# Kernel tuning notes

Hardware: AMD Instinct MI355X
Metric: run time of the kernel (lower is better)

Reference implementation:

```python
import jax, jax.numpy as jnp
import numpy as np

EMBED = 768
HEADS = 12


def setup_inputs() -> dict:
    key = jax.random.key(0)
    k1, k2, k3 = jax.random.split(key, 3)
    B, N, E = 2, 2048, EMBED
    x = jax.random.normal(k1, (B, N, E), dtype=jnp.float32)
    w_qkv = jax.random.normal(k2, (3 * E, E), dtype=jnp.float32) * (1.0 / np.sqrt(E))
    b_qkv = jnp.zeros((3 * E,), dtype=jnp.float32)
    w_o = jax.random.normal(k3, (E, E), dtype=jnp.float32) * (1.0 / np.sqrt(E))
    b_o = jnp.zeros((E,), dtype=jnp.float32)
    return {"x": x, "w_qkv": w_qkv, "b_qkv": b_qkv, "w_o": w_o, "b_o": b_o}


def reference(x, w_qkv, b_qkv, w_o, b_o):
    B, N, E = x.shape
    H = HEADS
    d = E // H
    # fused qkv projection (torch Linear: x @ W^T + b)
    qkv = x @ w_qkv.T + b_qkv                       # [B, N, 3E]
    # Rearrange 'b n (h qkv e) -> b qkv h n e'
    qkv = qkv.reshape(B, N, H, 3, d).transpose(0, 3, 2, 1, 4)  # [B, 3, H, N, d]
    q, k, v = qkv[:, 0], qkv[:, 1], qkv[:, 2]       # each [B, H, N, d]
    scores = jnp.einsum("bhqd,bhkd->bhqk", q, k)    # [B, H, N, N]
    attn = jax.nn.softmax(scores / jnp.sqrt(jnp.float32(E)), axis=-1)
    ctx = jnp.einsum("bhqk,bhkd->bhqd", attn, v)    # [B, H, N, d]
    ctx = ctx.transpose(0, 2, 1, 3).reshape(B, N, E)  # 'b h n d -> b n (h d)'
    out = ctx @ w_o.T + b_o
    return out
```

## Files before the change

### kernel.cpp

```cpp
#include <hip/hip_runtime.h>

#define BB 2
#define NN 2048
#define EE 768
#define HH 12
#define DD 64
#define MM (BB*NN)
#define E3 (3*EE)
#define QSCALE 0.05205877280961602f

typedef __bf16 bf16x8 __attribute__((ext_vector_type(8)));
typedef float  f32x4  __attribute__((ext_vector_type(4)));
typedef unsigned short u16x8 __attribute__((ext_vector_type(8)));

#define MFMA(a,b,c) __builtin_amdgcn_mfma_f32_16x16x32_bf16(a,b,c,0,0,0)

__device__ __forceinline__ unsigned short f2bf(float f) {
    unsigned int u = __float_as_uint(f);
    u += 0x7FFFu + ((u >> 16) & 1u);
    return (unsigned short)(u >> 16);
}

typedef __attribute__((address_space(3))) unsigned int as3u32;
typedef __attribute__((address_space(1))) unsigned int as1u32;
__device__ __forceinline__ void gll16(const void* g, void* l) {
    __builtin_amdgcn_global_load_lds((const as1u32*)(uintptr_t)g,
                                     (as3u32*)(unsigned int)(uintptr_t)l, 16, 0, 0);
}

__global__ __launch_bounds__(256)
void cast_bf16(const float* __restrict__ s, unsigned short* __restrict__ d, int n4) {
    int i = blockIdx.x * 256 + threadIdx.x;
    if (i < n4) {
        float4 v = ((const float4*)s)[i];
        ushort4 o;
        o.x = f2bf(v.x); o.y = f2bf(v.y); o.z = f2bf(v.z); o.w = f2bf(v.w);
        ((ushort4*)d)[i] = o;
    }
}

template<int MODE>
__global__ __launch_bounds__(256)
void gemm_bf16(const unsigned short* __restrict__ A, const unsigned short* __restrict__ W,
               const float* __restrict__ bias,
               unsigned short* __restrict__ o0, unsigned short* __restrict__ o1,
               unsigned short* __restrict__ o2, float* __restrict__ of, int Kd)
{
    __shared__ unsigned short As[128 * 32];
    __shared__ unsigned short Bs[128 * 32];

    const int tid = threadIdx.x;
    const int l = tid & 63;
    const int w = tid >> 6;
    const int m0 = blockIdx.x * 128;
    const int c0 = blockIdx.y * 128;
    const int wm = (w >> 1) * 64;
    const int wn = (w & 1) * 64;

    const int s0 = w * 2;
    const unsigned short* a_src0 = A + (size_t)(m0 + s0*16      + (l>>2)) * Kd + (l&3)*8;
    const unsigned short* a_src1 = A + (size_t)(m0 + (s0+1)*16  + (l>>2)) * Kd + (l&3)*8;
    const unsigned short* b_src0 = W + (size_t)(c0 + s0*16      + (l>>2)) * Kd + (l&3)*8;
    const unsigned short* b_src1 = W + (size_t)(c0 + (s0+1)*16  + (l>>2)) * Kd + (l&3)*8;
    unsigned short* a_dst0 = &As[s0*512];
    unsigned short* a_dst1 = &As[(s0+1)*512];
    unsigned short* b_dst0 = &Bs[s0*512];
    unsigned short* b_dst1 = &Bs[(s0+1)*512];

    const f32x4 zero4 = {0.f, 0.f, 0.f, 0.f};
    f32x4 acc[4][4];
    #pragma unroll
    for (int i = 0; i < 4; ++i)
        #pragma unroll
        for (int j = 0; j < 4; ++j) acc[i][j] = zero4;

    for (int k0 = 0; k0 < Kd; k0 += 32) {
        __syncthreads();
        gll16(a_src0 + k0, a_dst0);
        gll16(a_src1 + k0, a_dst1);
        gll16(b_src0 + k0, b_dst0);
        gll16(b_src1 + k0, b_dst1);
        __syncthreads();

        bf16x8 af[4], bf[4];
        #pragma unroll
        for (int i = 0; i < 4; ++i)
            af[i] = *(const bf16x8*)&As[(wm + 16*i + (l&15))*32 + (l>>4)*8];
        #pragma unroll
        for (int j = 0; j < 4; ++j)
            bf[j] = *(const bf16x8*)&Bs[(wn + 16*j + (l&15))*32 + (l>>4)*8];
        #pragma unroll
        for (int i = 0; i < 4; ++i)
            #pragma unroll
            for (int j = 0; j < 4; ++j)
                acc[i][j] = MFMA(af[i], bf[j], acc[i][j]);
    }

    if (MODE == 0) {
        #pragma unroll
        for (int j = 0; j < 4; ++j) {
            const int col = c0 + wn + 16*j + (l&15);
            const float bj = bias[col];
            #pragma unroll
            for (int i = 0; i < 4; ++i) {
                #pragma unroll
                for (int r = 0; r < 4; ++r) {
                    const int row = m0 + wm + 16*i + (l>>4)*4 + r;
                    of[(size_t)row * EE + col] = acc[i][j][r] + bj;
                }
            }
        }
    } else {
        const int sec = (c0 + wn) >> 6;
        const int hh = sec / 3;
        const int tt = sec - hh*3;
        #pragma unroll
        for (int j = 0; j < 4; ++j) {
            const int col = c0 + wn + 16*j + (l&15);
            const int dcol = 16*j + (l&15);
            const float bj = bias[col];
            #pragma unroll
            for (int i = 0; i < 4; ++i) {
                const int row0 = m0 + wm + 16*i + (l>>4)*4;
                const int b = row0 >> 11;
                const int n = row0 & (NN - 1);
                if (tt == 2) {
                    ushort4 pk;
                    pk.x = f2bf(acc[i][j][0] + bj);
                    pk.y = f2bf(acc[i][j][1] + bj);
                    pk.z = f2bf(acc[i][j][2] + bj);
                    pk.w = f2bf(acc[i][j][3] + bj);
                    *(ushort4*)&o2[(((size_t)b*HH + hh)*DD + dcol)*NN + n] = pk;
                } else {
                    unsigned short* dst = (tt == 0) ? o0 : o1;
                    #pragma unroll
                    for (int r = 0; r < 4; ++r) {
                        float val = acc[i][j][r] + bj;
                        if (tt == 0) val *= QSCALE;
                        dst[(((size_t)b*HH + hh)*NN + n + r)*DD + dcol] = f2bf(val);
                    }
                }
            }
        }
    }
}

__global__ __launch_bounds__(256)
void attn_mfma(const unsigned short* __restrict__ Q, const unsigned short* __restrict__ K,
               const unsigned short* __restrict__ Vt_g, unsigned short* __restrict__ ctx)
{
    __shared__ unsigned short Ks[64 * 72];
    __shared__ unsigned short Vt[64 * 72];
    __shared__ unsigned short Pq[4 * 16 * 72];

    const int tid = threadIdx.x;
    const int l = tid & 63;
    const int w = tid >> 6;
    const int quad = l >> 4;
    const int lc = l & 15;
    const int bq = blockIdx.x, h = blockIdx.y, b = blockIdx.z;
    const size_t hb = ((size_t)(b*HH + h)) * NN * DD;

    const f32x4 zero4 = {0.f, 0.f, 0.f, 0.f};

    const int qrow = bq*64 + w*16 + lc;
    const bf16x8 qf0 = *(const bf16x8*)(Q + hb + (size_t)qrow*DD +      quad*8);
    const bf16x8 qf1 = *(const bf16x8*)(Q + hb + (size_t)qrow*DD + 32 + quad*8);

    f32x4 o[4];
    #pragma unroll
    for (int dj = 0; dj < 4; ++dj) o[dj] = zero4;
    float lsum = 0.f;

    const int srow = tid >> 2;
    const int sc = tid & 3;
    const unsigned short* kbase = K + hb + (size_t)srow*DD + sc*16;
    const unsigned short* vbase = Vt_g + ((size_t)(b*HH + h)*DD + srow)*NN + sc*16;
    unsigned short* ksl = &Ks[srow*72 + sc*16];
    unsigned short* vsl = &Vt[srow*72 + sc*16];

    for (int kt = 0; kt < NN/64; ++kt) {
        const unsigned short* ksrc = kbase + (size_t)kt*64*DD;
        const unsigned short* vsrc = vbase + kt*64;
        u16x8 k0 = *(const u16x8*)ksrc;
        u16x8 k1 = *(const u16x8*)(ksrc + 8);
        u16x8 v0 = *(const u16x8*)vsrc;
        u16x8 v1 = *(const u16x8*)(vsrc + 8);
        __syncthreads();
        *(u16x8*)ksl = k0;
        *(u16x8*)(ksl + 8) = k1;
        *(u16x8*)vsl = v0;
        *(u16x8*)(vsl + 8) = v1;
        __syncthreads();

        f32x4 st[4];
        #pragma unroll
        for (int jf = 0; jf < 4; ++jf) {
            bf16x8 kf0 = *(const bf16x8*)&Ks[(16*jf + lc)*72 +      quad*8];
            bf16x8 kf1 = *(const bf16x8*)&Ks[(16*jf + lc)*72 + 32 + quad*8];
            f32x4 acc0 = MFMA(kf0, qf0, zero4);
            st[jf] = MFMA(kf1, qf1, acc0);
        }

        #pragma unroll
        for (int jf = 0; jf < 4; ++jf) {
            float e0 = __builtin_amdgcn_exp2f(st[jf][0]);
            float e1 = __builtin_amdgcn_exp2f(st[jf][1]);
            float e2 = __builtin_amdgcn_exp2f(st[jf][2]);
            float e3 = __builtin_amdgcn_exp2f(st[jf][3]);
            lsum += (e0 + e1) + (e2 + e3);
            ushort4 pk;
            pk.x = f2bf(e0); pk.y = f2bf(e1); pk.z = f2bf(e2); pk.w = f2bf(e3);
            *(ushort4*)&Pq[w*1152 + lc*72 + 16*jf + quad*4] = pk;
        }

        #pragma unroll
        for (int kb = 0; kb < 2; ++kb) {
            bf16x8 pf = *(const bf16x8*)&Pq[w*1152 + lc*72 + kb*32 + quad*8];
            #pragma unroll
            for (int dj = 0; dj < 4; ++dj) {
                bf16x8 vf = *(const bf16x8*)&Vt[(16*dj + lc)*72 + kb*32 + quad*8];
                o[dj] = MFMA(vf, pf, o[dj]);
            }
        }
    }

    lsum += __shfl_xor(lsum, 16);
    lsum += __shfl_xor(lsum, 32);
    const float inv = 1.f / lsum;

    const int n = bq*64 + w*16 + lc;
    #pragma unroll
    for (int dj = 0; dj < 4; ++dj) {
        ushort4 pk;
        pk.x = f2bf(o[dj][0] * inv);
        pk.y = f2bf(o[dj][1] * inv);
        pk.z = f2bf(o[dj][2] * inv);
        pk.w = f2bf(o[dj][3] * inv);
        *(ushort4*)&ctx[((size_t)(b*NN + n))*EE + h*DD + 16*dj + quad*4] = pk;
    }
}

extern "C" void kernel_launch(void* const* d_in, const int* in_sizes, int n_in,
                              void* d_out, int out_size, void* d_ws, size_t ws_size,
                              hipStream_t stream)
{
    const float* x     = (const float*)d_in[0];
    const float* w_qkv = (const float*)d_in[1];
    const float* b_qkv = (const float*)d_in[2];
    const float* w_o   = (const float*)d_in[3];
    const float* b_o   = (const float*)d_in[4];
    float* out = (float*)d_out;

    unsigned short* wsu = (unsigned short*)d_ws;
    const size_t XB = (size_t)MM * EE;
    const size_t WQ = (size_t)E3 * EE;
    const size_t WO = (size_t)EE * EE;
    const size_t HS = (size_t)BB * HH * NN * DD;
    unsigned short* xb   = wsu;
    unsigned short* wqb  = xb  + XB;
    unsigned short* wob  = wqb + WQ;
    unsigned short* qb   = wob + WO;
    unsigned short* kb   = qb  + HS;
    unsigned short* vtb  = kb  + HS;
    unsigned short* ctxb = vtb + HS;

    cast_bf16<<<(int)((XB/4 + 255)/256), 256, 0, stream>>>(x, xb, (int)(XB/4));
    cast_bf16<<<(int)((WQ/4 + 255)/256), 256, 0, stream>>>(w_qkv, wqb, (int)(WQ/4));
    cast_bf16<<<(int)((WO/4 + 255)/256), 256, 0, stream>>>(w_o, wob, (int)(WO/4));

    dim3 g1(MM/128, E3/128);
    gemm_bf16<1><<<g1, 256, 0, stream>>>(xb, wqb, b_qkv, qb, kb, vtb, nullptr, EE);

    dim3 g2(NN/64, HH, BB);
    attn_mfma<<<g2, 256, 0, stream>>>(qb, kb, vtb, ctxb);

    dim3 g3(MM/128, EE/128);
    gemm_bf16<0><<<g3, 256, 0, stream>>>(ctxb, wob, b_o, nullptr, nullptr, nullptr, out, EE);
}
```

Before: 180.3 us.

## Rewrite attention with 32x32 MFMA, register P shuffles, async LDS loads; fuse casts

Attention now uses 32x32x16 bf16 MFMA with 2 waves per 64-query block, each wave owning 32 queries. The probability tile is repacked to bf16 and passed between lanes with shuffles instead of a round-trip through shared memory. K and V tiles are staged with global_load_lds into XOR-swizzled LDS without padding, and the grid is flattened so the 24 batch-head pairs vary fastest. The three cast kernels are merged into one launch, which relies on xb, wqb and wob being contiguous in the workspace. Fewer threads per block reduce parallel loads, and the loads are still not double-buffered, so latency may stay exposed.

Result: slower. 237.9 us (+31.9%).

```diff
diff --git a/kernel.cpp b/kernel.cpp
--- a/kernel.cpp
+++ b/kernel.cpp
@@ -11,9 +11,12 @@
 
 typedef __bf16 bf16x8 __attribute__((ext_vector_type(8)));
 typedef float  f32x4  __attribute__((ext_vector_type(4)));
+typedef float  f32x16 __attribute__((ext_vector_type(16)));
 typedef unsigned short u16x8 __attribute__((ext_vector_type(8)));
-
-#define MFMA(a,b,c) __builtin_amdgcn_mfma_f32_16x16x32_bf16(a,b,c,0,0,0)
+typedef unsigned int   u32x4 __attribute__((ext_vector_type(4)));
+
+#define MFMA(a,b,c)   __builtin_amdgcn_mfma_f32_16x16x32_bf16(a,b,c,0,0,0)
+#define MFMA32(a,b,c) __builtin_amdgcn_mfma_f32_32x32x16_bf16(a,b,c,0,0,0)
 
 __device__ __forceinline__ unsigned short f2bf(float f) {
     unsigned int u = __float_as_uint(f);
@@ -28,15 +31,22 @@
                                      (as3u32*)(unsigned int)(uintptr_t)l, 16, 0, 0);
 }
 
+#define XB4 786432
+#define WQ4 442368
+#define WO4 147456
 __global__ __launch_bounds__(256)
-void cast_bf16(const float* __restrict__ s, unsigned short* __restrict__ d, int n4) {
+void cast3(const float* __restrict__ x, const float* __restrict__ wq,
+           const float* __restrict__ wo, unsigned short* __restrict__ dst) {
     int i = blockIdx.x * 256 + threadIdx.x;
-    if (i < n4) {
-        float4 v = ((const float4*)s)[i];
-        ushort4 o;
-        o.x = f2bf(v.x); o.y = f2bf(v.y); o.z = f2bf(v.z); o.w = f2bf(v.w);
-        ((ushort4*)d)[i] = o;
-    }
+    const float* src;
+    int off;
+    if (i < XB4)            { src = x;  off = i; }
+    else if (i < XB4+WQ4)   { src = wq; off = i - XB4; }
+    else                    { src = wo; off = i - XB4 - WQ4; }
+    float4 v = ((const float4*)src)[off];
+    ushort4 o;
+    o.x = f2bf(v.x); o.y = f2bf(v.y); o.z = f2bf(v.z); o.w = f2bf(v.w);
+    ((ushort4*)dst)[i] = o;
 }
 
 template<int MODE>
@@ -145,99 +155,115 @@
     }
 }
 
-__global__ __launch_bounds__(256)
+__global__ __launch_bounds__(128)
 void attn_mfma(const unsigned short* __restrict__ Q, const unsigned short* __restrict__ K,
                const unsigned short* __restrict__ Vt_g, unsigned short* __restrict__ ctx)
 {
-    __shared__ unsigned short Ks[64 * 72];
-    __shared__ unsigned short Vt[64 * 72];
-    __shared__ unsigned short Pq[4 * 16 * 72];
+    __shared__ unsigned short Ks[64 * 64];
+    __shared__ unsigned short Vt[64 * 64];
 
     const int tid = threadIdx.x;
-    const int l = tid & 63;
-    const int w = tid >> 6;
-    const int quad = l >> 4;
-    const int lc = l & 15;
-    const int bq = blockIdx.x, h = blockIdx.y, b = blockIdx.z;
-    const size_t hb = ((size_t)(b*HH + h)) * NN * DD;
-
-    const f32x4 zero4 = {0.f, 0.f, 0.f, 0.f};
-
-    const int qrow = bq*64 + w*16 + lc;
-    const bf16x8 qf0 = *(const bf16x8*)(Q + hb + (size_t)qrow*DD +      quad*8);
-    const bf16x8 qf1 = *(const bf16x8*)(Q + hb + (size_t)qrow*DD + 32 + quad*8);
-
-    f32x4 o[4];
+    const int l  = tid & 63;
+    const int wv = tid >> 6;
+    const int hf = l >> 5;
+    const int lc = l & 31;
+    const int l7 = l & 7;
+
+    const int id = blockIdx.x;
+    const int bh = id % 24;
+    const int qt = id / 24;
+    const int b  = bh / 12;
+    const int hh = bh - b*12;
+    const size_t hbK = (size_t)bh * NN * DD;
+
+    const f32x16 z16 = {0.f,0.f,0.f,0.f,0.f,0.f,0.f,0.f,
+                        0.f,0.f,0.f,0.f,0.f,0.f,0.f,0.f};
+
+    const int qbase = qt*64 + wv*32;
+    const unsigned short* qptr = Q + hbK + (size_t)(qbase + lc)*DD + hf*8;
+    bf16x8 qf[4];
     #pragma unroll
-    for (int dj = 0; dj < 4; ++dj) o[dj] = zero4;
+    for (int t = 0; t < 4; ++t) qf[t] = *(const bf16x8*)(qptr + t*16);
+
+    const int lr3 = l >> 3;
+    const int cx  = (l & 7) ^ (lr3 & 7);
+    const unsigned short* srcK0 = K   + hbK + (size_t)(32*wv + lr3)*DD + cx*8;
+    const unsigned short* srcV0 = Vt_g + ((size_t)bh*DD + 32*wv + lr3)*NN + cx*8;
+
+    f32x16 o0 = z16, o1 = z16;
     float lsum = 0.f;
 
-    const int srow = tid >> 2;
-    const int sc = tid & 3;
-    const unsigned short* kbase = K + hb + (size_t)srow*DD + sc*16;
-    const unsigned short* vbase = Vt_g + ((size_t)(b*HH + h)*DD + srow)*NN + sc*16;
-    unsigned short* ksl = &Ks[srow*72 + sc*16];
-    unsigned short* vsl = &Vt[srow*72 + sc*16];
-
     for (int kt = 0; kt < NN/64; ++kt) {
-        const unsigned short* ksrc = kbase + (size_t)kt*64*DD;
-        const unsigned short* vsrc = vbase + kt*64;
-        u16x8 k0 = *(const u16x8*)ksrc;
-        u16x8 k1 = *(const u16x8*)(ksrc + 8);
-        u16x8 v0 = *(const u16x8*)vsrc;
-        u16x8 v1 = *(const u16x8*)(vsrc + 8);
         __syncthreads();
-        *(u16x8*)ksl = k0;
-        *(u16x8*)(ksl + 8) = k1;
-        *(u16x8*)vsl = v0;
-        *(u16x8*)(vsl + 8) = v1;
+        const unsigned short* sk = srcK0 + (size_t)kt*64*DD;
+        const unsigned short* sv = srcV0 + kt*64;
+        #pragma unroll
+        for (int oo = 0; oo < 4; ++oo) {
+            gll16(sk + oo*8*DD, &Ks[(4*wv + oo)*512]);
+            gll16(sv + (size_t)oo*8*NN, &Vt[(4*wv + oo)*512]);
+        }
         __syncthreads();
 
-        f32x4 st[4];
-        #pragma unroll
-        for (int jf = 0; jf < 4; ++jf) {
-            bf16x8 kf0 = *(const bf16x8*)&Ks[(16*jf + lc)*72 +      quad*8];
-            bf16x8 kf1 = *(const bf16x8*)&Ks[(16*jf + lc)*72 + 32 + quad*8];
-            f32x4 acc0 = MFMA(kf0, qf0, zero4);
-            st[jf] = MFMA(kf1, qf1, acc0);
-        }
-
-        #pragma unroll
-        for (int jf = 0; jf < 4; ++jf) {
-            float e0 = __builtin_amdgcn_exp2f(st[jf][0]);
-            float e1 = __builtin_amdgcn_exp2f(st[jf][1]);
-            float e2 = __builtin_amdgcn_exp2f(st[jf][2]);
-            float e3 = __builtin_amdgcn_exp2f(st[jf][3]);
+        f32x16 st0 = z16, st1 = z16;
+        #pragma unroll
+        for (int t = 0; t < 4; ++t) {
+            const int ch = ((2*t + hf) ^ l7) * 8;
+            bf16x8 kf0 = *(const bf16x8*)&Ks[(     lc)*64 + ch];
+            bf16x8 kf1 = *(const bf16x8*)&Ks[(32 + lc)*64 + ch];
+            st0 = MFMA32(kf0, qf[t], st0);
+            st1 = MFMA32(kf1, qf[t], st1);
+        }
+
+        unsigned int pk[2][8];
+        #pragma unroll
+        for (int m = 0; m < 8; ++m) {
+            float e0 = __builtin_amdgcn_exp2f(st0[2*m]);
+            float e1 = __builtin_amdgcn_exp2f(st0[2*m+1]);
+            float e2 = __builtin_amdgcn_exp2f(st1[2*m]);
+            float e3 = __builtin_amdgcn_exp2f(st1[2*m+1]);
             lsum += (e0 + e1) + (e2 + e3);
-            ushort4 pk;
-            pk.x = f2bf(e0); pk.y = f2bf(e1); pk.z = f2bf(e2); pk.w = f2bf(e3);
-            *(ushort4*)&Pq[w*1152 + lc*72 + 16*jf + quad*4] = pk;
-        }
-
-        #pragma unroll
-        for (int kb = 0; kb < 2; ++kb) {
-            bf16x8 pf = *(const bf16x8*)&Pq[w*1152 + lc*72 + kb*32 + quad*8];
-            #pragma unroll
-            for (int dj = 0; dj < 4; ++dj) {
-                bf16x8 vf = *(const bf16x8*)&Vt[(16*dj + lc)*72 + kb*32 + quad*8];
-                o[dj] = MFMA(vf, pf, o[dj]);
-            }
+            pk[0][m] = __builtin_amdgcn_perm(__float_as_uint(e1) + 0x8000u,
+                                             __float_as_uint(e0) + 0x8000u, 0x07060302u);
+            pk[1][m] = __builtin_amdgcn_perm(__float_as_uint(e3) + 0x8000u,
+                                             __float_as_uint(e2) + 0x8000u, 0x07060302u);
+        }
+
+        #pragma unroll
+        for (int s = 0; s < 4; ++s) {
+            const int kb = s >> 1;
+            const int m0 = 4*(s & 1) + 2*hf;
+            const unsigned int p0 = pk[kb][m0];
+            const unsigned int p1 = pk[kb][m0 + 1];
+            const unsigned int x0 = __shfl_xor(pk[kb][m0 ^ 2], 32);
+            const unsigned int x1 = __shfl_xor(pk[kb][(m0 ^ 2) + 1], 32);
+            u32x4 fr;
+            fr[0] = hf ? x0 : p0;
+            fr[1] = hf ? x1 : p1;
+            fr[2] = hf ? p0 : x0;
+            fr[3] = hf ? p1 : x1;
+            bf16x8 pf = __builtin_bit_cast(bf16x8, fr);
+            const int ch = ((2*s + hf) ^ l7) * 8;
+            bf16x8 vf0 = *(const bf16x8*)&Vt[(     lc)*64 + ch];
+            bf16x8 vf1 = *(const bf16x8*)&Vt[(32 + lc)*64 + ch];
+            o0 = MFMA32(vf0, pf, o0);
+            o1 = MFMA32(vf1, pf, o1);
         }
     }
 
-    lsum += __shfl_xor(lsum, 16);
     lsum += __shfl_xor(lsum, 32);
     const float inv = 1.f / lsum;
 
-    const int n = bq*64 + w*16 + lc;
+    const int qg = qbase + lc;
+    unsigned short* cp = ctx + ((size_t)(b*NN + qg))*EE + hh*DD;
     #pragma unroll
-    for (int dj = 0; dj < 4; ++dj) {
-        ushort4 pk;
-        pk.x = f2bf(o[dj][0] * inv);
-        pk.y = f2bf(o[dj][1] * inv);
-        pk.z = f2bf(o[dj][2] * inv);
-        pk.w = f2bf(o[dj][3] * inv);
-        *(ushort4*)&ctx[((size_t)(b*NN + n))*EE + h*DD + 16*dj + quad*4] = pk;
+    for (int g = 0; g < 4; ++g) {
+        ushort4 pa, pb;
+        pa.x = f2bf(o0[4*g+0]*inv); pa.y = f2bf(o0[4*g+1]*inv);
+        pa.z = f2bf(o0[4*g+2]*inv); pa.w = f2bf(o0[4*g+3]*inv);
+        pb.x = f2bf(o1[4*g+0]*inv); pb.y = f2bf(o1[4*g+1]*inv);
+        pb.z = f2bf(o1[4*g+2]*inv); pb.w = f2bf(o1[4*g+3]*inv);
+        *(ushort4*)(cp +      8*g + 4*hf) = pa;
+        *(ushort4*)(cp + 32 + 8*g + 4*hf) = pb;
     }
 }
 
@@ -265,15 +291,12 @@
     unsigned short* vtb  = kb  + HS;
     unsigned short* ctxb = vtb + HS;
 
-    cast_bf16<<<(int)((XB/4 + 255)/256), 256, 0, stream>>>(x, xb, (int)(XB/4));
-    cast_bf16<<<(int)((WQ/4 + 255)/256), 256, 0, stream>>>(w_qkv, wqb, (int)(WQ/4));
-    cast_bf16<<<(int)((WO/4 + 255)/256), 256, 0, stream>>>(w_o, wob, (int)(WO/4));
+    cast3<<<(XB4 + WQ4 + WO4)/256, 256, 0, stream>>>(x, w_qkv, w_o, xb);
 
     dim3 g1(MM/128, E3/128);
     gemm_bf16<1><<<g1, 256, 0, stream>>>(xb, wqb, b_qkv, qb, kb, vtb, nullptr, EE);
 
-    dim3 g2(NN/64, HH, BB);
-    attn_mfma<<<g2, 256, 0, stream>>>(qb, kb, vtb, ctxb);
+    attn_mfma<<<768, 128, 0, stream>>>(qb, kb, vtb, ctxb);
 
     dim3 g3(MM/128, EE/128);
     gemm_bf16<0><<<g3, 256, 0, stream>>>(ctxb, wob, b_o, nullptr, nullptr, nullptr, out, EE);
```
